# Kernel tuning notes

Measured on AMD Instinct MI355X. Metric: run time of the kernel, lower is better.

The kernel has to match this reference:

```python
import jax, jax.numpy as jnp
import numpy as np

INPUT_SIZE = 4
HIDDEN_SIZE = 64
OUTPUT_SIZE = 40
BATCH = 4096
SEQ_LEN = 512


def setup_inputs() -> dict:
    key = jax.random.key(0)
    ks = jax.random.split(key, 7)
    s_ih = 1.0 / np.sqrt(HIDDEN_SIZE)
    x = jax.random.normal(ks[0], (BATCH, SEQ_LEN, INPUT_SIZE), dtype=jnp.float32)
    # PyTorch nn.RNN params, uniform(-1/sqrt(H), 1/sqrt(H))
    W_ih = jax.random.uniform(ks[1], (HIDDEN_SIZE, INPUT_SIZE), minval=-s_ih, maxval=s_ih, dtype=jnp.float32)
    W_hh = jax.random.uniform(ks[2], (HIDDEN_SIZE, HIDDEN_SIZE), minval=-s_ih, maxval=s_ih, dtype=jnp.float32)
    b_ih = jax.random.uniform(ks[3], (HIDDEN_SIZE,), minval=-s_ih, maxval=s_ih, dtype=jnp.float32)
    b_hh = jax.random.uniform(ks[4], (HIDDEN_SIZE,), minval=-s_ih, maxval=s_ih, dtype=jnp.float32)
    fc_W = jax.random.uniform(ks[5], (OUTPUT_SIZE, HIDDEN_SIZE), minval=-s_ih, maxval=s_ih, dtype=jnp.float32)
    fc_b = jax.random.uniform(ks[6], (OUTPUT_SIZE,), minval=-s_ih, maxval=s_ih, dtype=jnp.float32)
    return {"x": x, "W_ih": W_ih, "W_hh": W_hh, "b_ih": b_ih, "b_hh": b_hh, "fc_W": fc_W, "fc_b": fc_b}


def reference(x, W_ih, W_hh, b_ih, b_hh, fc_W, fc_b):
    B = x.shape[0]
    # Precompute input projections for all timesteps: [T, B, H]
    xp = jnp.einsum('bti,hi->tbh', x, W_ih) + (b_ih + b_hh)

    def step(h, xp_t):
        h = jnp.tanh(xp_t + h @ W_hh.T)
        return h, None

    h0 = jnp.zeros((B, HIDDEN_SIZE), dtype=x.dtype)
    h_last, _ = jax.lax.scan(step, h0, xp)
    # fc on last timestep hidden state
    return h_last @ fc_W.T + fc_b
```

## Files before the change

### kernel.cpp

```cpp
#include <hip/hip_runtime.h>
#include <math.h>

#define BATCH 4096
#define SEQ_T 512
#define ISZ   4
#define HID   64
#define OSZ   40
#define RPB   16

typedef __attribute__((ext_vector_type(8))) _Float16     half8;
typedef __attribute__((ext_vector_type(2))) _Float16     half2v;
typedef __attribute__((ext_vector_type(4))) float        float4v;
typedef __attribute__((ext_vector_type(2))) unsigned int uint2v;

static __device__ __forceinline__ half2v pk_f16(float a, float b) {
    return __builtin_bit_cast(half2v, __builtin_amdgcn_cvt_pkrtz(a, b));
}

static __device__ __forceinline__ float fast_tanh(float x) {
    float e = __expf(2.0f * x);
    return 1.0f - 2.0f * __builtin_amdgcn_rcpf(e + 1.0f);
}

__global__ __launch_bounds__(256, 1)
void rnn_f16x2_kernel(const float* __restrict__ x,
                      const float* __restrict__ W_ih,
                      const float* __restrict__ W_hh,
                      const float* __restrict__ b_ih,
                      const float* __restrict__ b_hh,
                      const float* __restrict__ fc_W,
                      const float* __restrict__ fc_b,
                      float* __restrict__ out)
{
    __shared__ __attribute__((aligned(16))) _Float16 hterm[2][2][8][16][8];
    __shared__ __attribute__((aligned(16))) float hf[16][68];

    const int tid  = threadIdx.x;
    const int wv   = tid >> 6;
    const int lane = tid & 63;
    const int n    = lane & 15;
    const int q    = lane >> 4;
    const int blk0 = blockIdx.x * RPB;

    {
        unsigned int* p = (unsigned int*)hterm;
        #pragma unroll
        for (int i = tid; i < (int)(sizeof(hterm) / 4); i += 256) p[i] = 0u;
    }

    half8 A10, A11, A20, A21;
    {
        const float* wr = W_hh + (16 * wv + n) * HID;
        #pragma unroll
        for (int j = 0; j < 8; ++j) {
            float f0 = wr[     8 * q + j];
            float f1 = wr[32 + 8 * q + j];
            _Float16 h0 = (_Float16)f0; A10[j] = h0; A20[j] = (_Float16)(f0 - (float)h0);
            _Float16 h1 = (_Float16)f1; A11[j] = h1; A21[j] = (_Float16)(f1 - (float)h1);
        }
    }

    const int r0 = 16 * wv + 4 * q;
    float wih[4][4], bias[4];
    #pragma unroll
    for (int r = 0; r < 4; ++r) {
        bias[r] = b_ih[r0 + r] + b_hh[r0 + r];
        #pragma unroll
        for (int i = 0; i < ISZ; ++i) wih[r][i] = W_ih[(r0 + r) * ISZ + i];
    }

    const float* xrow = x + (size_t)(blk0 + n) * SEQ_T * ISZ;
    float4v xcur = *(const float4v*)(xrow);
    float4v xnxt = *(const float4v*)(xrow + ISZ);

    const int gw = 2 * wv + (q >> 1);
    const int j0 = 4 * (q & 1);

    float hl0 = 0.f, hl1 = 0.f, hl2 = 0.f, hl3 = 0.f;

    __syncthreads();

#define MFMA16(A, B, C) __builtin_amdgcn_mfma_f32_16x16x32_f16((A), (B), (C), 0, 0, 0)
#define RNN_STEP(RB, WB, T)                                                    \
    {                                                                          \
        int tn = (T) + 2; if (tn > SEQ_T - 1) tn = SEQ_T - 1;                  \
        const float4v xf = *(const float4v*)(xrow + (size_t)tn * ISZ);         \
        half8 B10 = *(const half8*)&hterm[RB][0][    q][n][0];                 \
        half8 B11 = *(const half8*)&hterm[RB][0][4 + q][n][0];                 \
        half8 B20 = *(const half8*)&hterm[RB][1][    q][n][0];                 \
        half8 B21 = *(const half8*)&hterm[RB][1][4 + q][n][0];                 \
        float p0 = bias[0], p1 = bias[1], p2 = bias[2], p3 = bias[3];          \
        _Pragma("unroll")                                                      \
        for (int i = 0; i < ISZ; ++i) {                                        \
            p0 = fmaf(xcur[i], wih[0][i], p0);                                 \
            p1 = fmaf(xcur[i], wih[1][i], p1);                                 \
            p2 = fmaf(xcur[i], wih[2][i], p2);                                 \
            p3 = fmaf(xcur[i], wih[3][i], p3);                                 \
        }                                                                      \
        float4v accA = {p0, p1, p2, p3};                                       \
        float4v accB = {0.f, 0.f, 0.f, 0.f};                                   \
        accA = MFMA16(A10, B10, accA);  accB = MFMA16(A11, B11, accB);         \
        accA = MFMA16(A10, B20, accA);  accB = MFMA16(A11, B21, accB);         \
        accA = MFMA16(A20, B10, accA);  accB = MFMA16(A21, B11, accB);         \
        hl0 = fast_tanh(accA[0] + accB[0]); hl1 = fast_tanh(accA[1] + accB[1]);\
        hl2 = fast_tanh(accA[2] + accB[2]); hl3 = fast_tanh(accA[3] + accB[3]);\
        half2v hi01 = pk_f16(hl0, hl1), hi23 = pk_f16(hl2, hl3);               \
        float s0 = hl0 - (float)hi01[0], s1 = hl1 - (float)hi01[1];            \
        float s2 = hl2 - (float)hi23[0], s3 = hl3 - (float)hi23[1];            \
        half2v lo01 = pk_f16(s0, s1), lo23 = pk_f16(s2, s3);                   \
        uint2v whi = { __builtin_bit_cast(unsigned int, hi01),                 \
                       __builtin_bit_cast(unsigned int, hi23) };               \
        uint2v wlo = { __builtin_bit_cast(unsigned int, lo01),                 \
                       __builtin_bit_cast(unsigned int, lo23) };               \
        *(uint2v*)&hterm[WB][0][gw][n][j0] = whi;                              \
        *(uint2v*)&hterm[WB][1][gw][n][j0] = wlo;                              \
        xcur = xnxt; xnxt = xf;                                                \
        __syncthreads();                                                       \
    }

    for (int t = 0; t < SEQ_T; t += 2) {
        RNN_STEP(0, 1, t)
        RNN_STEP(1, 0, t + 1)
    }
#undef RNN_STEP
#undef MFMA16

    {
        float4v hv = {hl0, hl1, hl2, hl3};
        *(float4v*)&hf[n][16 * wv + 4 * q] = hv;
    }
    __syncthreads();
    for (int it = tid; it < RPB * OSZ; it += 256) {
        const int b = it / OSZ;
        const int o = it - b * OSZ;
        const float* wo = fc_W + o * HID;
        float acc = fc_b[o];
        #pragma unroll
        for (int j = 0; j < HID; ++j)
            acc = fmaf(hf[b][j], wo[j], acc);
        out[(size_t)(blk0 + b) * OSZ + o] = acc;
    }
}

extern "C" void kernel_launch(void* const* d_in, const int* in_sizes, int n_in,
                              void* d_out, int out_size, void* d_ws, size_t ws_size,
                              hipStream_t stream) {
    const float* x    = (const float*)d_in[0];
    const float* W_ih = (const float*)d_in[1];
    const float* W_hh = (const float*)d_in[2];
    const float* b_ih = (const float*)d_in[3];
    const float* b_hh = (const float*)d_in[4];
    const float* fc_W = (const float*)d_in[5];
    const float* fc_b = (const float*)d_in[6];
    float* out = (float*)d_out;

    rnn_f16x2_kernel<<<BATCH / RPB, 256, 0, stream>>>(
        x, W_ih, W_hh, b_ih, b_hh, fc_W, fc_b, out);
}
```

Before: 230.8 us.

## Stage input chunks in LDS with cooperative prefetch instead of per-step global loads

Replaces the per-timestep global load of x (each lane reading 16 bytes strided by row, with a two-step register prefetch) with cooperative loads of 32-timestep chunks. Each thread loads two float4s per chunk, stores them to LDS, and prefetches the next chunk into registers. The recurrent steps then read x from LDS, which takes global memory latency off the serial recurrence path. In exchange it adds an LDS buffer, one extra barrier per chunk and extra LDS reads per step, and unrolls the inner 32-step loop, which increases code size.

```diff
diff --git a/kernel.cpp b/kernel.cpp
--- a/kernel.cpp
+++ b/kernel.cpp
@@ -7,6 +7,8 @@
 #define HID   64
 #define OSZ   40
 #define RPB   16
+#define CHNK  32
+#define NCH   (SEQ_T / CHNK)
 
 typedef __attribute__((ext_vector_type(8))) _Float16     half8;
 typedef __attribute__((ext_vector_type(2))) _Float16     half2v;
@@ -23,16 +25,17 @@
 }
 
 __global__ __launch_bounds__(256, 1)
-void rnn_f16x2_kernel(const float* __restrict__ x,
-                      const float* __restrict__ W_ih,
-                      const float* __restrict__ W_hh,
-                      const float* __restrict__ b_ih,
-                      const float* __restrict__ b_hh,
-                      const float* __restrict__ fc_W,
-                      const float* __restrict__ fc_b,
-                      float* __restrict__ out)
+void rnn_f16x2s_kernel(const float* __restrict__ x,
+                       const float* __restrict__ W_ih,
+                       const float* __restrict__ W_hh,
+                       const float* __restrict__ b_ih,
+                       const float* __restrict__ b_hh,
+                       const float* __restrict__ fc_W,
+                       const float* __restrict__ fc_b,
+                       float* __restrict__ out)
 {
     __shared__ __attribute__((aligned(16))) _Float16 hterm[2][2][8][16][8];
+    __shared__ __attribute__((aligned(16))) float xlds[CHNK][17][4];
     __shared__ __attribute__((aligned(16))) float hf[16][68];
 
     const int tid  = threadIdx.x;
@@ -69,22 +72,21 @@
         for (int i = 0; i < ISZ; ++i) wih[r][i] = W_ih[(r0 + r) * ISZ + i];
     }
 
-    const float* xrow = x + (size_t)(blk0 + n) * SEQ_T * ISZ;
-    float4v xcur = *(const float4v*)(xrow);
-    float4v xnxt = *(const float4v*)(xrow + ISZ);
+    const int sn = tid >> 4;
+    const int st = (tid & 15) * 2;
+    const float* xsrc = x + ((size_t)(blk0 + sn) * SEQ_T + st) * ISZ;
+    float4v xr0 = *(const float4v*)(xsrc);
+    float4v xr1 = *(const float4v*)(xsrc + 4);
 
     const int gw = 2 * wv + (q >> 1);
     const int j0 = 4 * (q & 1);
 
     float hl0 = 0.f, hl1 = 0.f, hl2 = 0.f, hl3 = 0.f;
 
-    __syncthreads();
-
 #define MFMA16(A, B, C) __builtin_amdgcn_mfma_f32_16x16x32_f16((A), (B), (C), 0, 0, 0)
-#define RNN_STEP(RB, WB, T)                                                    \
+#define RNN_STEP(RB, WB, S)                                                    \
     {                                                                          \
-        int tn = (T) + 2; if (tn > SEQ_T - 1) tn = SEQ_T - 1;                  \
-        const float4v xf = *(const float4v*)(xrow + (size_t)tn * ISZ);         \
+        const float4v xv = *(const float4v*)&xlds[S][n][0];                    \
         half8 B10 = *(const half8*)&hterm[RB][0][    q][n][0];                 \
         half8 B11 = *(const half8*)&hterm[RB][0][4 + q][n][0];                 \
         half8 B20 = *(const half8*)&hterm[RB][1][    q][n][0];                 \
@@ -92,10 +94,10 @@
         float p0 = bias[0], p1 = bias[1], p2 = bias[2], p3 = bias[3];          \
         _Pragma("unroll")                                                      \
         for (int i = 0; i < ISZ; ++i) {                                        \
-            p0 = fmaf(xcur[i], wih[0][i], p0);                                 \
-            p1 = fmaf(xcur[i], wih[1][i], p1);                                 \
-            p2 = fmaf(xcur[i], wih[2][i], p2);                                 \
-            p3 = fmaf(xcur[i], wih[3][i], p3);                                 \
+            p0 = fmaf(xv[i], wih[0][i], p0);                                   \
+            p1 = fmaf(xv[i], wih[1][i], p1);                                   \
+            p2 = fmaf(xv[i], wih[2][i], p2);                                   \
+            p3 = fmaf(xv[i], wih[3][i], p3);                                   \
         }                                                                      \
         float4v accA = {p0, p1, p2, p3};                                       \
         float4v accB = {0.f, 0.f, 0.f, 0.f};                                   \
@@ -114,13 +116,23 @@
                        __builtin_bit_cast(unsigned int, lo23) };               \
         *(uint2v*)&hterm[WB][0][gw][n][j0] = whi;                              \
         *(uint2v*)&hterm[WB][1][gw][n][j0] = wlo;                              \
-        xcur = xnxt; xnxt = xf;                                                \
         __syncthreads();                                                       \
     }
 
-    for (int t = 0; t < SEQ_T; t += 2) {
-        RNN_STEP(0, 1, t)
-        RNN_STEP(1, 0, t + 1)
+    for (int c = 0; c < NCH; ++c) {
+        *(float4v*)&xlds[st    ][sn][0] = xr0;
+        *(float4v*)&xlds[st + 1][sn][0] = xr1;
+        const int cn = (c + 1 < NCH) ? c + 1 : NCH - 1;
+        const float* p = x + ((size_t)(blk0 + sn) * SEQ_T + cn * CHNK + st) * ISZ;
+        xr0 = *(const float4v*)(p);
+        xr1 = *(const float4v*)(p + 4);
+        __syncthreads();
+
+        #pragma unroll
+        for (int s = 0; s < CHNK; s += 2) {
+            RNN_STEP(0, 1, s)
+            RNN_STEP(1, 0, s + 1)
+        }
     }
 #undef RNN_STEP
 #undef MFMA16
@@ -154,6 +166,6 @@
     const float* fc_b = (const float*)d_in[6];
     float* out = (float*)d_out;
 
-    rnn_f16x2_kernel<<<BATCH / RPB, 256, 0, stream>>>(
+    rnn_f16x2s_kernel<<<BATCH / RPB, 256, 0, stream>>>(
         x, W_ih, W_hh, b_ih, b_hh, fc_W, fc_b, out);
 }
```

Result: slower. 245.0 us (+6.2%).

## Compute two RNN steps per barrier with redundant full-state step per wave

Applied to the files above, without the earlier changes.

Each wave now redundantly computes the full 64-wide hidden state for the first of two timesteps into a private LDS buffer, then computes its own 16-row slice of the second step. This halves the number of block-wide barriers per sequence. The input projection and bias are folded into an extra MFMA through split-f16 x values and an augmented weight fragment. The cost is four times the MFMA and tanh work on the first step and many more live registers.

```diff
diff --git a/kernel.cpp b/kernel.cpp
--- a/kernel.cpp
+++ b/kernel.cpp
@@ -16,23 +16,23 @@
 static __device__ __forceinline__ half2v pk_f16(float a, float b) {
     return __builtin_bit_cast(half2v, __builtin_amdgcn_cvt_pkrtz(a, b));
 }
-
 static __device__ __forceinline__ float fast_tanh(float x) {
     float e = __expf(2.0f * x);
     return 1.0f - 2.0f * __builtin_amdgcn_rcpf(e + 1.0f);
 }
 
 __global__ __launch_bounds__(256, 1)
-void rnn_f16x2_kernel(const float* __restrict__ x,
-                      const float* __restrict__ W_ih,
-                      const float* __restrict__ W_hh,
-                      const float* __restrict__ b_ih,
-                      const float* __restrict__ b_hh,
-                      const float* __restrict__ fc_W,
-                      const float* __restrict__ fc_b,
-                      float* __restrict__ out)
+void rnn_pair_kernel(const float* __restrict__ x,
+                     const float* __restrict__ W_ih,
+                     const float* __restrict__ W_hh,
+                     const float* __restrict__ b_ih,
+                     const float* __restrict__ b_hh,
+                     const float* __restrict__ fc_W,
+                     const float* __restrict__ fc_b,
+                     float* __restrict__ out)
 {
-    __shared__ __attribute__((aligned(16))) _Float16 hterm[2][2][8][16][8];
+    __shared__ __attribute__((aligned(16))) _Float16 hsh[2][2][8][16][8];
+    __shared__ __attribute__((aligned(16))) _Float16 hpv[4][2][8][16][8];
     __shared__ __attribute__((aligned(16))) float hf[16][68];
 
     const int tid  = threadIdx.x;
@@ -41,69 +41,154 @@
     const int n    = lane & 15;
     const int q    = lane >> 4;
     const int blk0 = blockIdx.x * RPB;
+    const int j0   = 4 * (q & 1);
 
     {
-        unsigned int* p = (unsigned int*)hterm;
-        #pragma unroll
-        for (int i = tid; i < (int)(sizeof(hterm) / 4); i += 256) p[i] = 0u;
-    }
-
-    half8 A10, A11, A20, A21;
+        unsigned int* p = (unsigned int*)hsh;
+        #pragma unroll
+        for (int i = tid; i < (int)(sizeof(hsh) / 4); i += 256) p[i] = 0u;
+    }
+
+    half8 A1c0[4], A1c1[4], A2c0[4], A2c1[4], A3[4];
+    #pragma unroll
+    for (int g = 0; g < 4; ++g) {
+        const float* wr = W_hh + (16 * g + n) * HID;
+        #pragma unroll
+        for (int j = 0; j < 8; ++j) {
+            float f0 = wr[     8 * q + j];
+            float f1 = wr[32 + 8 * q + j];
+            _Float16 h0 = (_Float16)f0; A1c0[g][j] = h0; A2c0[g][j] = (_Float16)(f0 - (float)h0);
+            _Float16 h1 = (_Float16)f1; A1c1[g][j] = h1; A2c1[g][j] = (_Float16)(f1 - (float)h1);
+        }
+        float wf0 = W_ih[(16*g+n)*4+0], wf1 = W_ih[(16*g+n)*4+1];
+        float wf2 = W_ih[(16*g+n)*4+2], wf3 = W_ih[(16*g+n)*4+3];
+        float bs  = b_ih[16*g+n] + b_hh[16*g+n];
+        _Float16 bh = (_Float16)bs;
+        _Float16 bl = (_Float16)(bs - (float)bh);
+        #pragma unroll
+        for (int j = 0; j < 8; ++j) {
+            float w = (j&3)==0 ? wf0 : (j&3)==1 ? wf1 : (j&3)==2 ? wf2 : wf3;
+            _Float16 whi = (_Float16)w;
+            _Float16 wlo = (_Float16)(w - (float)whi);
+            _Float16 v = (_Float16)0.0f;
+            if (q == 0) v = whi;
+            else if (q == 1) v = (j < 4) ? wlo : (j == 4) ? bh : (j == 5) ? bl : (_Float16)0.0f;
+            A3[g][j] = v;
+        }
+    }
+    half8 AB1c0, AB1c1, AB2c0, AB2c1, AB3;
     {
         const float* wr = W_hh + (16 * wv + n) * HID;
         #pragma unroll
         for (int j = 0; j < 8; ++j) {
             float f0 = wr[     8 * q + j];
             float f1 = wr[32 + 8 * q + j];
-            _Float16 h0 = (_Float16)f0; A10[j] = h0; A20[j] = (_Float16)(f0 - (float)h0);
-            _Float16 h1 = (_Float16)f1; A11[j] = h1; A21[j] = (_Float16)(f1 - (float)h1);
-        }
-    }
-
-    const int r0 = 16 * wv + 4 * q;
-    float wih[4][4], bias[4];
-    #pragma unroll
-    for (int r = 0; r < 4; ++r) {
-        bias[r] = b_ih[r0 + r] + b_hh[r0 + r];
-        #pragma unroll
-        for (int i = 0; i < ISZ; ++i) wih[r][i] = W_ih[(r0 + r) * ISZ + i];
+            _Float16 h0 = (_Float16)f0; AB1c0[j] = h0; AB2c0[j] = (_Float16)(f0 - (float)h0);
+            _Float16 h1 = (_Float16)f1; AB1c1[j] = h1; AB2c1[j] = (_Float16)(f1 - (float)h1);
+        }
+        float wf0 = W_ih[(16*wv+n)*4+0], wf1 = W_ih[(16*wv+n)*4+1];
+        float wf2 = W_ih[(16*wv+n)*4+2], wf3 = W_ih[(16*wv+n)*4+3];
+        float bs  = b_ih[16*wv+n] + b_hh[16*wv+n];
+        _Float16 bh = (_Float16)bs;
+        _Float16 bl = (_Float16)(bs - (float)bh);
+        #pragma unroll
+        for (int j = 0; j < 8; ++j) {
+            float w = (j&3)==0 ? wf0 : (j&3)==1 ? wf1 : (j&3)==2 ? wf2 : wf3;
+            _Float16 whi = (_Float16)w;
+            _Float16 wlo = (_Float16)(w - (float)whi);
+            _Float16 v = (_Float16)0.0f;
+            if (q == 0) v = whi;
+            else if (q == 1) v = (j < 4) ? wlo : (j == 4) ? bh : (j == 5) ? bl : (_Float16)0.0f;
+            AB3[j] = v;
+        }
     }
 
     const float* xrow = x + (size_t)(blk0 + n) * SEQ_T * ISZ;
-    float4v xcur = *(const float4v*)(xrow);
-    float4v xnxt = *(const float4v*)(xrow + ISZ);
-
-    const int gw = 2 * wv + (q >> 1);
-    const int j0 = 4 * (q & 1);
+    float4v xc0 = *(const float4v*)(xrow);
+    float4v xc1 = *(const float4v*)(xrow + ISZ);
 
     float hl0 = 0.f, hl1 = 0.f, hl2 = 0.f, hl3 = 0.f;
 
+    const unsigned int ONE2 = 0x3C003C00u;
+
     __syncthreads();
 
 #define MFMA16(A, B, C) __builtin_amdgcn_mfma_f32_16x16x32_f16((A), (B), (C), 0, 0, 0)
-#define RNN_STEP(RB, WB, T)                                                    \
+#define BUILD_B3(DST, XV)                                                      \
     {                                                                          \
-        int tn = (T) + 2; if (tn > SEQ_T - 1) tn = SEQ_T - 1;                  \
-        const float4v xf = *(const float4v*)(xrow + (size_t)tn * ISZ);         \
-        half8 B10 = *(const half8*)&hterm[RB][0][    q][n][0];                 \
-        half8 B11 = *(const half8*)&hterm[RB][0][4 + q][n][0];                 \
-        half8 B20 = *(const half8*)&hterm[RB][1][    q][n][0];                 \
-        half8 B21 = *(const half8*)&hterm[RB][1][4 + q][n][0];                 \
-        float p0 = bias[0], p1 = bias[1], p2 = bias[2], p3 = bias[3];          \
+        half2v xh01 = pk_f16((XV)[0], (XV)[1]), xh23 = pk_f16((XV)[2], (XV)[3]); \
+        float l0 = (XV)[0] - (float)xh01[0], l1 = (XV)[1] - (float)xh01[1];    \
+        float l2 = (XV)[2] - (float)xh23[0], l3 = (XV)[3] - (float)xh23[1];    \
+        half2v xl01 = pk_f16(l0, l1), xl23 = pk_f16(l2, l3);                   \
+        unsigned int uh01 = __builtin_bit_cast(unsigned int, xh01);            \
+        unsigned int uh23 = __builtin_bit_cast(unsigned int, xh23);            \
+        unsigned int ul01 = __builtin_bit_cast(unsigned int, xl01);            \
+        unsigned int ul23 = __builtin_bit_cast(unsigned int, xl23);            \
+        unsigned int d0 = (q < 2) ? uh01 : 0u;                                 \
+        unsigned int d1 = (q < 2) ? uh23 : 0u;                                 \
+        unsigned int d2 = (q == 0) ? ul01 : (q == 1) ? ONE2 : 0u;              \
+        unsigned int d3 = (q == 0) ? ul23 : 0u;                                \
+        unsigned int tmp[4] = {d0, d1, d2, d3};                                \
+        DST = *(half8*)tmp;                                                    \
+    }
+
+#define PAIR(RB, WB, P)                                                        \
+    {                                                                          \
+        int t2 = 2*(P) + 2; if (t2 > SEQ_T - 1) t2 = SEQ_T - 1;                \
+        int t3 = 2*(P) + 3; if (t3 > SEQ_T - 1) t3 = SEQ_T - 1;                \
+        const float4v xf0 = *(const float4v*)(xrow + (size_t)t2 * ISZ);        \
+        const float4v xf1 = *(const float4v*)(xrow + (size_t)t3 * ISZ);        \
+                     \
+        half8 B10 = *(const half8*)&hsh[RB][0][    q][n][0];                   \
+        half8 B11 = *(const half8*)&hsh[RB][0][4 + q][n][0];                   \
+        half8 B20 = *(const half8*)&hsh[RB][1][    q][n][0];                   \
+        half8 B21 = *(const half8*)&hsh[RB][1][4 + q][n][0];                   \
+        half8 B3a; BUILD_B3(B3a, xc0)                                          \
         _Pragma("unroll")                                                      \
-        for (int i = 0; i < ISZ; ++i) {                                        \
-            p0 = fmaf(xcur[i], wih[0][i], p0);                                 \
-            p1 = fmaf(xcur[i], wih[1][i], p1);                                 \
-            p2 = fmaf(xcur[i], wih[2][i], p2);                                 \
-            p3 = fmaf(xcur[i], wih[3][i], p3);                                 \
+        for (int g = 0; g < 4; ++g) {                                          \
+            float4v aA = {0.f, 0.f, 0.f, 0.f};                                 \
+            float4v aB = {0.f, 0.f, 0.f, 0.f};                                 \
+            aB = MFMA16(A3[g],   B3a, aB);                                     \
+            aA = MFMA16(A1c0[g], B10, aA);                                     \
+            aB = MFMA16(A1c1[g], B11, aB);                                     \
+            aA = MFMA16(A1c0[g], B20, aA);                                     \
+            aB = MFMA16(A1c1[g], B21, aB);                                     \
+            aA = MFMA16(A2c0[g], B10, aA);                                     \
+            aB = MFMA16(A2c1[g], B11, aB);                                     \
+            float v0 = fast_tanh(aA[0] + aB[0]);                               \
+            float v1 = fast_tanh(aA[1] + aB[1]);                               \
+            float v2 = fast_tanh(aA[2] + aB[2]);                               \
+            float v3 = fast_tanh(aA[3] + aB[3]);                               \
+            half2v hi01 = pk_f16(v0, v1), hi23 = pk_f16(v2, v3);               \
+            float s0 = v0 - (float)hi01[0], s1 = v1 - (float)hi01[1];          \
+            float s2 = v2 - (float)hi23[0], s3 = v3 - (float)hi23[1];          \
+            half2v lo01 = pk_f16(s0, s1), lo23 = pk_f16(s2, s3);               \
+            uint2v whi = { __builtin_bit_cast(unsigned int, hi01),             \
+                           __builtin_bit_cast(unsigned int, hi23) };           \
+            uint2v wlo = { __builtin_bit_cast(unsigned int, lo01),             \
+                           __builtin_bit_cast(unsigned int, lo23) };           \
+            *(uint2v*)&hpv[wv][0][2*g + (q >> 1)][n][j0] = whi;                \
+            *(uint2v*)&hpv[wv][1][2*g + (q >> 1)][n][j0] = wlo;                \
         }                                                                      \
-        float4v accA = {p0, p1, p2, p3};                                       \
-        float4v accB = {0.f, 0.f, 0.f, 0.f};                                   \
-        accA = MFMA16(A10, B10, accA);  accB = MFMA16(A11, B11, accB);         \
-        accA = MFMA16(A10, B20, accA);  accB = MFMA16(A11, B21, accB);         \
-        accA = MFMA16(A20, B10, accA);  accB = MFMA16(A21, B11, accB);         \
-        hl0 = fast_tanh(accA[0] + accB[0]); hl1 = fast_tanh(accA[1] + accB[1]);\
-        hl2 = fast_tanh(accA[2] + accB[2]); hl3 = fast_tanh(accA[3] + accB[3]);\
+         \
+        half8 C10 = *(const half8*)&hpv[wv][0][    q][n][0];                   \
+        half8 C11 = *(const half8*)&hpv[wv][0][4 + q][n][0];                   \
+        half8 C20 = *(const half8*)&hpv[wv][1][    q][n][0];                   \
+        half8 C21 = *(const half8*)&hpv[wv][1][4 + q][n][0];                   \
+        half8 B3b; BUILD_B3(B3b, xc1)                                          \
+        float4v aA = {0.f, 0.f, 0.f, 0.f};                                     \
+        float4v aB = {0.f, 0.f, 0.f, 0.f};                                     \
+        aB = MFMA16(AB3,   B3b, aB);                                           \
+        aA = MFMA16(AB1c0, C10, aA);                                           \
+        aB = MFMA16(AB1c1, C11, aB);                                           \
+        aA = MFMA16(AB1c0, C20, aA);                                           \
+        aB = MFMA16(AB1c1, C21, aB);                                           \
+        aA = MFMA16(AB2c0, C10, aA);                                           \
+        aB = MFMA16(AB2c1, C11, aB);                                           \
+        hl0 = fast_tanh(aA[0] + aB[0]);                                        \
+        hl1 = fast_tanh(aA[1] + aB[1]);                                        \
+        hl2 = fast_tanh(aA[2] + aB[2]);                                        \
+        hl3 = fast_tanh(aA[3] + aB[3]);                                        \
         half2v hi01 = pk_f16(hl0, hl1), hi23 = pk_f16(hl2, hl3);               \
         float s0 = hl0 - (float)hi01[0], s1 = hl1 - (float)hi01[1];            \
         float s2 = hl2 - (float)hi23[0], s3 = hl3 - (float)hi23[1];            \
@@ -112,17 +197,18 @@
                        __builtin_bit_cast(unsigned int, hi23) };               \
         uint2v wlo = { __builtin_bit_cast(unsigned int, lo01),                 \
                        __builtin_bit_cast(unsigned int, lo23) };               \
-        *(uint2v*)&hterm[WB][0][gw][n][j0] = whi;                              \
-        *(uint2v*)&hterm[WB][1][gw][n][j0] = wlo;                              \
-        xcur = xnxt; xnxt = xf;                                                \
+        *(uint2v*)&hsh[WB][0][2*wv + (q >> 1)][n][j0] = whi;                   \
+        *(uint2v*)&hsh[WB][1][2*wv + (q >> 1)][n][j0] = wlo;                   \
+        xc0 = xf0; xc1 = xf1;                                                  \
         __syncthreads();                                                       \
     }
 
-    for (int t = 0; t < SEQ_T; t += 2) {
-        RNN_STEP(0, 1, t)
-        RNN_STEP(1, 0, t + 1)
-    }
-#undef RNN_STEP
+    for (int p = 0; p < SEQ_T / 2; p += 2) {
+        PAIR(0, 1, p)
+        PAIR(1, 0, p + 1)
+    }
+#undef PAIR
+#undef BUILD_B3
 #undef MFMA16
 
     {
@@ -154,6 +240,6 @@
     const float* fc_b = (const float*)d_in[6];
     float* out = (float*)d_out;
 
-    rnn_f16x2_kernel<<<BATCH / RPB, 256, 0, stream>>>(
+    rnn_pair_kernel<<<BATCH / RPB, 256, 0, stream>>>(
         x, W_ih, W_hh, b_ih, b_hh, fc_W, fc_b, out);
 }
```

Result: slower. 347.3 us (+50.5%).

## Process two independent 16-row tiles per block to interleave recurrent chains

Applied to the files above, without the earlier changes.

Each block now handles 32 batch rows as two independent 16-row tiles, running both tiles' MFMA/tanh chains back-to-back before a single barrier per timestep. This aims to hide the serial dependency latency of one tile behind the other and to halve barrier count per row. It halves the number of blocks, leaving only half of the CUs busy, and doubles shared-memory and register use per block.

```diff
diff --git a/kernel.cpp b/kernel.cpp
--- a/kernel.cpp
+++ b/kernel.cpp
@@ -6,7 +6,7 @@
 #define ISZ   4
 #define HID   64
 #define OSZ   40
-#define RPB   16
+#define RPB   32
 
 typedef __attribute__((ext_vector_type(8))) _Float16     half8;
 typedef __attribute__((ext_vector_type(2))) _Float16     half2v;
@@ -16,24 +16,23 @@
 static __device__ __forceinline__ half2v pk_f16(float a, float b) {
     return __builtin_bit_cast(half2v, __builtin_amdgcn_cvt_pkrtz(a, b));
 }
-
 static __device__ __forceinline__ float fast_tanh(float x) {
     float e = __expf(2.0f * x);
     return 1.0f - 2.0f * __builtin_amdgcn_rcpf(e + 1.0f);
 }
 
 __global__ __launch_bounds__(256, 1)
-void rnn_f16x2_kernel(const float* __restrict__ x,
-                      const float* __restrict__ W_ih,
-                      const float* __restrict__ W_hh,
-                      const float* __restrict__ b_ih,
-                      const float* __restrict__ b_hh,
-                      const float* __restrict__ fc_W,
-                      const float* __restrict__ fc_b,
-                      float* __restrict__ out)
+void rnn_dual_kernel(const float* __restrict__ x,
+                     const float* __restrict__ W_ih,
+                     const float* __restrict__ W_hh,
+                     const float* __restrict__ b_ih,
+                     const float* __restrict__ b_hh,
+                     const float* __restrict__ fc_W,
+                     const float* __restrict__ fc_b,
+                     float* __restrict__ out)
 {
-    __shared__ __attribute__((aligned(16))) _Float16 hterm[2][2][8][16][8];
-    __shared__ __attribute__((aligned(16))) float hf[16][68];
+    __shared__ __attribute__((aligned(16))) _Float16 hterm[2][2][2][8][16][8];
+    __shared__ __attribute__((aligned(16))) float hf[2][16][68];
 
     const int tid  = threadIdx.x;
     const int wv   = tid >> 6;
@@ -69,75 +68,91 @@
         for (int i = 0; i < ISZ; ++i) wih[r][i] = W_ih[(r0 + r) * ISZ + i];
     }
 
-    const float* xrow = x + (size_t)(blk0 + n) * SEQ_T * ISZ;
-    float4v xcur = *(const float4v*)(xrow);
-    float4v xnxt = *(const float4v*)(xrow + ISZ);
+    const float* xrowA = x + (size_t)(blk0      + n) * SEQ_T * ISZ;
+    const float* xrowB = x + (size_t)(blk0 + 16 + n) * SEQ_T * ISZ;
+    float4v xcurA = *(const float4v*)(xrowA);
+    float4v xnxtA = *(const float4v*)(xrowA + ISZ);
+    float4v xcurB = *(const float4v*)(xrowB);
+    float4v xnxtB = *(const float4v*)(xrowB + ISZ);
 
     const int gw = 2 * wv + (q >> 1);
     const int j0 = 4 * (q & 1);
 
-    float hl0 = 0.f, hl1 = 0.f, hl2 = 0.f, hl3 = 0.f;
+    float hlA0 = 0.f, hlA1 = 0.f, hlA2 = 0.f, hlA3 = 0.f;
+    float hlB0 = 0.f, hlB1 = 0.f, hlB2 = 0.f, hlB3 = 0.f;
 
     __syncthreads();
 
 #define MFMA16(A, B, C) __builtin_amdgcn_mfma_f32_16x16x32_f16((A), (B), (C), 0, 0, 0)
-#define RNN_STEP(RB, WB, T)                                                    \
+#define TILE_BODY(TI, SUF, RB, WB, T)                                          \
     {                                                                          \
         int tn = (T) + 2; if (tn > SEQ_T - 1) tn = SEQ_T - 1;                  \
-        const float4v xf = *(const float4v*)(xrow + (size_t)tn * ISZ);         \
-        half8 B10 = *(const half8*)&hterm[RB][0][    q][n][0];                 \
-        half8 B11 = *(const half8*)&hterm[RB][0][4 + q][n][0];                 \
-        half8 B20 = *(const half8*)&hterm[RB][1][    q][n][0];                 \
-        half8 B21 = *(const half8*)&hterm[RB][1][4 + q][n][0];                 \
+        const float4v xf = *(const float4v*)(xrow##SUF + (size_t)tn * ISZ);    \
+        half8 B10 = *(const half8*)&hterm[TI][RB][0][    q][n][0];             \
+        half8 B11 = *(const half8*)&hterm[TI][RB][0][4 + q][n][0];             \
+        half8 B20 = *(const half8*)&hterm[TI][RB][1][    q][n][0];             \
+        half8 B21 = *(const half8*)&hterm[TI][RB][1][4 + q][n][0];             \
         float p0 = bias[0], p1 = bias[1], p2 = bias[2], p3 = bias[3];          \
         _Pragma("unroll")                                                      \
         for (int i = 0; i < ISZ; ++i) {                                        \
-            p0 = fmaf(xcur[i], wih[0][i], p0);                                 \
-            p1 = fmaf(xcur[i], wih[1][i], p1);                                 \
-            p2 = fmaf(xcur[i], wih[2][i], p2);                                 \
-            p3 = fmaf(xcur[i], wih[3][i], p3);                                 \
+            p0 = fmaf(xcur##SUF[i], wih[0][i], p0);                            \
+            p1 = fmaf(xcur##SUF[i], wih[1][i], p1);                            \
+            p2 = fmaf(xcur##SUF[i], wih[2][i], p2);                            \
+            p3 = fmaf(xcur##SUF[i], wih[3][i], p3);                            \
         }                                                                      \
         float4v accA = {p0, p1, p2, p3};                                       \
         float4v accB = {0.f, 0.f, 0.f, 0.f};                                   \
         accA = MFMA16(A10, B10, accA);  accB = MFMA16(A11, B11, accB);         \
         accA = MFMA16(A10, B20, accA);  accB = MFMA16(A11, B21, accB);         \
         accA = MFMA16(A20, B10, accA);  accB = MFMA16(A21, B11, accB);         \
-        hl0 = fast_tanh(accA[0] + accB[0]); hl1 = fast_tanh(accA[1] + accB[1]);\
-        hl2 = fast_tanh(accA[2] + accB[2]); hl3 = fast_tanh(accA[3] + accB[3]);\
-        half2v hi01 = pk_f16(hl0, hl1), hi23 = pk_f16(hl2, hl3);               \
-        float s0 = hl0 - (float)hi01[0], s1 = hl1 - (float)hi01[1];            \
-        float s2 = hl2 - (float)hi23[0], s3 = hl3 - (float)hi23[1];            \
+        hl##SUF##0 = fast_tanh(accA[0] + accB[0]);                             \
+        hl##SUF##1 = fast_tanh(accA[1] + accB[1]);                             \
+        hl##SUF##2 = fast_tanh(accA[2] + accB[2]);                             \
+        hl##SUF##3 = fast_tanh(accA[3] + accB[3]);                             \
+        half2v hi01 = pk_f16(hl##SUF##0, hl##SUF##1);                          \
+        half2v hi23 = pk_f16(hl##SUF##2, hl##SUF##3);                          \
+        float s0 = hl##SUF##0 - (float)hi01[0], s1 = hl##SUF##1 - (float)hi01[1]; \
+        float s2 = hl##SUF##2 - (float)hi23[0], s3 = hl##SUF##3 - (float)hi23[1]; \
         half2v lo01 = pk_f16(s0, s1), lo23 = pk_f16(s2, s3);                   \
         uint2v whi = { __builtin_bit_cast(unsigned int, hi01),                 \
                        __builtin_bit_cast(unsigned int, hi23) };               \
         uint2v wlo = { __builtin_bit_cast(unsigned int, lo01),                 \
                        __builtin_bit_cast(unsigned int, lo23) };               \
-        *(uint2v*)&hterm[WB][0][gw][n][j0] = whi;                              \
-        *(uint2v*)&hterm[WB][1][gw][n][j0] = wlo;                              \
-        xcur = xnxt; xnxt = xf;                                                \
-        __syncthreads();                                                       \
+        *(uint2v*)&hterm[TI][WB][0][gw][n][j0] = whi;                          \
+        *(uint2v*)&hterm[TI][WB][1][gw][n][j0] = wlo;                          \
+        xcur##SUF = xnxt##SUF; xnxt##SUF = xf;                                 \
     }
+
+#define RNN_STEP(RB, WB, T)                                                    \
+    TILE_BODY(0, A, RB, WB, T)                                                 \
+    TILE_BODY(1, B, RB, WB, T)                                                 \
+    __syncthreads();
 
     for (int t = 0; t < SEQ_T; t += 2) {
         RNN_STEP(0, 1, t)
         RNN_STEP(1, 0, t + 1)
     }
 #undef RNN_STEP
+#undef TILE_BODY
 #undef MFMA16
 
     {
-        float4v hv = {hl0, hl1, hl2, hl3};
-        *(float4v*)&hf[n][16 * wv + 4 * q] = hv;
+        float4v hvA = {hlA0, hlA1, hlA2, hlA3};
+        float4v hvB = {hlB0, hlB1, hlB2, hlB3};
+        *(float4v*)&hf[0][n][16 * wv + 4 * q] = hvA;
+        *(float4v*)&hf[1][n][16 * wv + 4 * q] = hvB;
     }
     __syncthreads();
     for (int it = tid; it < RPB * OSZ; it += 256) {
-        const int b = it / OSZ;
-        const int o = it - b * OSZ;
+        const int b  = it / OSZ;
+        const int o  = it - b * OSZ;
+        const int ti = b >> 4;
+        const int bb = b & 15;
         const float* wo = fc_W + o * HID;
         float acc = fc_b[o];
         #pragma unroll
         for (int j = 0; j < HID; ++j)
-            acc = fmaf(hf[b][j], wo[j], acc);
+            acc = fmaf(hf[ti][bb][j], wo[j], acc);
         out[(size_t)(blk0 + b) * OSZ + o] = acc;
     }
 }
@@ -154,6 +169,6 @@
     const float* fc_b = (const float*)d_in[6];
     float* out = (float*)d_out;
 
-    rnn_f16x2_kernel<<<BATCH / RPB, 256, 0, stream>>>(
+    rnn_dual_kernel<<<BATCH / RPB, 256, 0, stream>>>(
         x, W_ih, W_hh, b_ih, b_hh, fc_W, fc_b, out);
 }
```

New measurement: 343.3 us. 1.49x slower.
